# Kernel tuning notes

Hardware: AMD Instinct MI355X
Metric: run time of the kernel (lower is better)

## Reference

```python
import jax, jax.numpy as jnp
import numpy as np

ALPHA = 1.5      # entmax alpha (q parameter)
N_ITER = 50      # entmax-bisect iterations (entmax library default)
B, S, DM, H, HKV, HD = 1, 2048, 2048, 16, 4, 128
ROPE_THETA = 10000.0


def _entmax_p(x):
    """alpha-entmax along last axis via bisection on tau (matches entmax.EntmaxBisect)."""
    am1 = ALPHA - 1.0
    pw = 1.0 / am1
    X = x * am1
    d = x.shape[-1]
    max_val = jnp.max(X, axis=-1, keepdims=True)
    tau_lo = max_val - 1.0                      # _gp(1, alpha) = 1
    tau_hi = max_val - (1.0 / d) ** am1          # _gp(1/d, alpha)
    dm0 = tau_hi - tau_lo

    def body(i, carry):
        tau_lo, dm, tau_m = carry
        dm = dm * 0.5
        tau_m = tau_lo + dm
        p = jnp.maximum(X - tau_m, 0.0) ** pw
        f = jnp.sum(p, axis=-1, keepdims=True) - 1.0
        tau_lo = jnp.where(f >= 0, tau_m, tau_lo)
        return (tau_lo, dm, tau_m)

    tau_lo, dm, tau_m = jax.lax.fori_loop(0, N_ITER, body, (tau_lo, dm0, tau_lo))
    p = jnp.maximum(X - tau_m, 0.0) ** pw
    return p / jnp.sum(p, axis=-1, keepdims=True)  # ensure_sum_one


@jax.custom_vjp
def entmax_bisect(x):
    return _entmax_p(x)

def _emx_fwd(x):
    p = _entmax_p(x)
    return p, p

def _emx_bwd(p, g):
    # entmax library backward: gppr = p^(2-alpha) on support
    gppr = jnp.where(p > 0, p ** (2.0 - ALPHA), 0.0)
    dX = g * gppr
    q = jnp.sum(dX, axis=-1, keepdims=True) / jnp.sum(gppr, axis=-1, keepdims=True)
    return ((dX - q * gppr),)

entmax_bisect.defvjp(_emx_fwd, _emx_bwd)


def _rotate_half(x):
    x1, x2 = x[..., : HD // 2], x[..., HD // 2:]
    return jnp.concatenate([-x2, x1], axis=-1)


def setup_inputs() -> dict:
    key = jax.random.key(0)
    k1, k2, k3, k4, k5 = jax.random.split(key, 5)
    hidden_states = jax.random.normal(k1, (B, S, DM), dtype=jnp.float32)
    wq = jax.random.normal(k2, (H * HD, DM), dtype=jnp.float32) * 0.02
    wk = jax.random.normal(k3, (HKV * HD, DM), dtype=jnp.float32) * 0.02
    wv = jax.random.normal(k4, (HKV * HD, DM), dtype=jnp.float32) * 0.02
    wo = jax.random.normal(k5, (DM, H * HD), dtype=jnp.float32) * 0.02
    # real Llama RoPE position embeddings
    inv_freq = 1.0 / (ROPE_THETA ** (np.arange(0, HD, 2, dtype=np.float32) / HD))
    pos = np.arange(S, dtype=np.float32)
    freqs = pos[:, None] * inv_freq[None, :]          # [S, HD/2]
    emb = np.concatenate([freqs, freqs], axis=-1)     # [S, HD]
    cos = jnp.asarray(np.cos(emb))[None]              # [1, S, HD]
    sin = jnp.asarray(np.sin(emb))[None]
    return {"hidden_states": hidden_states, "cos": cos, "sin": sin,
            "wq": wq, "wk": wk, "wv": wv, "wo": wo}


def reference(hidden_states, cos, sin, wq, wk, wv, wo):
    b, s, _ = hidden_states.shape
    scaling = HD ** -0.5
    # QKV projections -> [B, H, S, HD]
    q = (hidden_states @ wq.T).reshape(b, s, H, HD).transpose(0, 2, 1, 3)
    k = (hidden_states @ wk.T).reshape(b, s, HKV, HD).transpose(0, 2, 1, 3)
    v = (hidden_states @ wv.T).reshape(b, s, HKV, HD).transpose(0, 2, 1, 3)
    # RoPE (cos/sin broadcast over head axis)
    c, sn = cos[:, None, :, :], sin[:, None, :, :]
    q = q * c + _rotate_half(q) * sn
    k = k * c + _rotate_half(k) * sn
    # GQA: repeat kv heads
    g = H // HKV
    k = jnp.repeat(k, g, axis=1)
    v = jnp.repeat(v, g, axis=1)
    scores = jnp.einsum('bhqd,bhkd->bhqk', q, k) * scaling
    causal = jnp.tril(jnp.ones((s, s), dtype=bool))
    scores = jnp.where(causal, scores, -jnp.inf)
    attn = entmax_bisect(scores)                      # [B, H, S, S]
    out = jnp.einsum('bhqk,bhkd->bhqd', attn, v)
    out = out.transpose(0, 2, 1, 3).reshape(b, s, H * HD)
    out = out @ wo.T
    return (out, attn)
```

## Files before the change

### kernel.cpp

```cpp
#include <hip/hip_runtime.h>

typedef __bf16 bf16;
typedef __bf16 bf16x4 __attribute__((ext_vector_type(4)));
typedef __bf16 bf16x8 __attribute__((ext_vector_type(8)));
typedef float f32x4 __attribute__((ext_vector_type(4)));

#define S 2048
#define DM 2048
#define HD 128
#define H 16
#define NQKV 3072
#define N_ITER_DEV 32

__device__ __forceinline__ void gl2lds16(const void* g, void* l) {
    __builtin_amdgcn_global_load_lds(
        (const __attribute__((address_space(1))) void*)g,
        (__attribute__((address_space(3))) void*)l, 16, 0, 0);
}

__global__ void cvt_all(const float* __restrict__ hid, const float* __restrict__ wq,
                        const float* __restrict__ wk, const float* __restrict__ wv,
                        const float* __restrict__ wo, bf16* __restrict__ bh,
                        bf16* __restrict__ bqkv, bf16* __restrict__ bwo) {
    int i = blockIdx.x * blockDim.x + threadIdx.x;
    const float* src;
    bf16* dst;
    int off;
    if (i < 1048576) { src = hid; dst = bh; off = i; }
    else if (i < 2097152) { src = wq; dst = bqkv; off = i - 1048576; }
    else if (i < 2359296) { src = wk; dst = bqkv + 2048 * 2048; off = i - 2097152; }
    else if (i < 2621440) { src = wv; dst = bqkv + 2048 * 2048 + 512 * 2048; off = i - 2359296; }
    else { src = wo; dst = bwo; off = i - 2621440; }
    float4 f = ((const float4*)src)[off];
    bf16x4 o;
    o[0] = (bf16)f.x; o[1] = (bf16)f.y; o[2] = (bf16)f.z; o[3] = (bf16)f.w;
    ((bf16x4*)dst)[off] = o;
}

__global__ __launch_bounds__(256) void gemm128_bt(const bf16* __restrict__ A,
                                                  const bf16* __restrict__ B,
                                                  float* __restrict__ C, int Ndim, int K) {
    __shared__ bf16 As[128 * 32];
    __shared__ bf16 Bs[128 * 32];
    int m0 = blockIdx.x * 128, n0 = blockIdx.y * 128;
    int t = threadIdx.x;
    int l = t & 63, w = t >> 6;
    int lane16 = l & 15, quad = l >> 4;

    int c0 = (w * 2) * 64 + l;
    int c1 = c0 + 64;
    const bf16* Abase = A + (size_t)m0 * K;
    const bf16* Bbase = B + (size_t)n0 * K;

    int wm = (w & 1) * 64, wn = (w >> 1) * 64;
    f32x4 acc[4][4];
#pragma unroll
    for (int i = 0; i < 4; i++)
#pragma unroll
        for (int j = 0; j < 4; j++) acc[i][j] = (f32x4){0.f, 0.f, 0.f, 0.f};

    for (int k0 = 0; k0 < K; k0 += 32) {
        gl2lds16(Abase + (size_t)(c0 >> 2) * K + k0 + (c0 & 3) * 8, &As[(w * 2) * 512]);
        gl2lds16(Abase + (size_t)(c1 >> 2) * K + k0 + (c1 & 3) * 8, &As[(w * 2 + 1) * 512]);
        gl2lds16(Bbase + (size_t)(c0 >> 2) * K + k0 + (c0 & 3) * 8, &Bs[(w * 2) * 512]);
        gl2lds16(Bbase + (size_t)(c1 >> 2) * K + k0 + (c1 & 3) * 8, &Bs[(w * 2 + 1) * 512]);
        __syncthreads();
        bf16x8 af[4], bfr[4];
#pragma unroll
        for (int i = 0; i < 4; i++)
            af[i] = *(const bf16x8*)&As[(wm + i * 16 + lane16) * 32 + quad * 8];
#pragma unroll
        for (int j = 0; j < 4; j++)
            bfr[j] = *(const bf16x8*)&Bs[(wn + j * 16 + lane16) * 32 + quad * 8];
#pragma unroll
        for (int i = 0; i < 4; i++)
#pragma unroll
            for (int j = 0; j < 4; j++)
                acc[i][j] = __builtin_amdgcn_mfma_f32_16x16x32_bf16(af[i], bfr[j], acc[i][j], 0, 0, 0);
        __syncthreads();
    }
#pragma unroll
    for (int i = 0; i < 4; i++)
#pragma unroll
        for (int j = 0; j < 4; j++) {
            float* cp = C + (size_t)(m0 + wm + i * 16 + quad * 4) * Ndim + n0 + wn + j * 16 + lane16;
#pragma unroll
            for (int r = 0; r < 4; r++) cp[(size_t)r * Ndim] = acc[i][j][r];
        }
}

__global__ void rope_kernel(const float* __restrict__ qkv, const float* __restrict__ cosb,
                            const float* __restrict__ sinb, bf16* __restrict__ qs,
                            bf16* __restrict__ kb, bf16* __restrict__ vT) {
    int col = blockIdx.x * 256 + threadIdx.x;
    int s = blockIdx.y;
    const float* row = qkv + (size_t)s * NQKV;
    float v = row[col];
    if (col < DM) {
        int h = col >> 7, d = col & 127;
        float c = cosb[s * HD + d], sn = sinb[s * HD + d];
        float other = row[(h << 7) + ((d < 64) ? (d + 64) : (d - 64))];
        float rot = (d < 64) ? -other : other;
        float o = v * c + rot * sn;
        qs[((size_t)h * S + s) * HD + d] = (bf16)(o * 0.04419417382415922f);
    } else if (col < DM + 512) {
        int c2 = col - DM;
        int kv = c2 >> 7, d = c2 & 127;
        float c = cosb[s * HD + d], sn = sinb[s * HD + d];
        float other = row[DM + (kv << 7) + ((d < 64) ? (d + 64) : (d - 64))];
        float rot = (d < 64) ? -other : other;
        float o = v * c + rot * sn;
        kb[((size_t)kv * S + s) * HD + d] = (bf16)o;
    } else {
        int c2 = col - DM - 512;
        int kv = c2 >> 7, d = c2 & 127;
        vT[((size_t)kv * HD + d) * S + s] = (bf16)v;
    }
}

template <int SEGS>
__global__ __launch_bounds__(1024) void attn_av_kernel(const bf16* __restrict__ qs,
                                                       const bf16* __restrict__ kb,
                                                       const bf16* __restrict__ vT,
                                                       float* __restrict__ attn,
                                                       bf16* __restrict__ o, int bx_base) {
    constexpr int NREG = SEGS * 8;
    __shared__ float sc[16][528];
    __shared__ bf16 pb[16][552];
    int bx = bx_base + blockIdx.x;
    int h = blockIdx.y;
    int r0 = bx * 16;
    int jlen = r0 + 16;
    int l = threadIdx.x & 63;
    int w = threadIdx.x >> 6;
    int lane16 = l & 15, quad = l >> 4;

    const bf16* qrow = qs + ((size_t)h * S + (r0 + lane16)) * HD + quad * 8;
    bf16x8 afrag[4];
#pragma unroll
    for (int kc = 0; kc < 4; kc++) afrag[kc] = *(const bf16x8*)(qrow + kc * 32);

    const bf16* kbase = kb + (size_t)(h >> 2) * S * HD;
    const bf16* vbase = vT + (size_t)(h >> 2) * HD * S;
    float xr[NREG];
    int my_i = r0 + w;

#pragma unroll
    for (int sgi = 0; sgi < SEGS; sgi++) {
        int j0 = sgi * 512;
#pragma unroll
        for (int tt = 0; tt < 2; tt++) {
            int t = w + tt * 16;
            int jt = j0 + t * 16;
            if (jt < jlen) {
                f32x4 acc = {0.f, 0.f, 0.f, 0.f};
                const bf16* kp = kbase + (size_t)(jt + lane16) * HD + quad * 8;
#pragma unroll
                for (int kc = 0; kc < 4; kc++) {
                    bf16x8 b = *(const bf16x8*)(kp + kc * 32);
                    acc = __builtin_amdgcn_mfma_f32_16x16x32_bf16(afrag[kc], b, acc, 0, 0, 0);
                }
                int jj = jt + lane16;
#pragma unroll
                for (int r = 0; r < 4; r++) {
                    int rowi = quad * 4 + r;
                    float v = acc[r];
                    if (jj > r0 + rowi) v = -1e30f;
                    sc[rowi][t * 16 + lane16] = v;
                }
            }
        }
        __syncthreads();
#pragma unroll
        for (int c = 0; c < 8; c++) {
            int j = j0 + c * 64 + l;
            xr[sgi * 8 + c] = (j < jlen) ? sc[w][c * 64 + l] : -1e30f;
        }
        __syncthreads();
    }

    float m = -1e30f;
#pragma unroll
    for (int c = 0; c < NREG; c++) m = fmaxf(m, xr[c]);
#pragma unroll
    for (int off = 1; off < 64; off <<= 1) m = fmaxf(m, __shfl_xor(m, off));

    float tau_lo = m - 1.0f;
    float dmh = 0.97790291309f;
    float tau_m = tau_lo;
    for (int it = 0; it < N_ITER_DEV; it++) {
        dmh *= 0.5f;
        tau_m = tau_lo + dmh;
        float f = 0.f;
#pragma unroll
        for (int c = 0; c < NREG; c++) {
            float t = fmaxf(xr[c] - tau_m, 0.f);
            f = fmaf(t, t, f);
        }
#pragma unroll
        for (int off = 1; off < 64; off <<= 1) f += __shfl_xor(f, off);
        tau_lo = (f >= 1.0f) ? tau_m : tau_lo;
    }

    float ssum = 0.f;
#pragma unroll
    for (int c = 0; c < NREG; c++) {
        float t = fmaxf(xr[c] - tau_m, 0.f);
        ssum = fmaf(t, t, ssum);
    }
#pragma unroll
    for (int off = 1; off < 64; off <<= 1) ssum += __shfl_xor(ssum, off);
    float inv = 1.0f / ssum;

    float* arow = attn + ((size_t)h * S + my_i) * S;
    int jt_o = (w & 7) * 16;
    int kh = (w >> 3) * 256;
    f32x4 acc_o = {0.f, 0.f, 0.f, 0.f};

#pragma unroll
    for (int sgi = 0; sgi < SEGS; sgi++) {
        int j0 = sgi * 512;
#pragma unroll
        for (int c = 0; c < 8; c++) {
            float t = fmaxf(xr[sgi * 8 + c] - tau_m, 0.f);
            float p = t * t * inv;
            arow[j0 + c * 64 + l] = p;
            pb[w][c * 64 + l] = (bf16)p;
        }
        __syncthreads();
#pragma unroll
        for (int ks = 0; ks < 8; ks++) {
            int kk = kh + ks * 32;
            bf16x8 a = *(const bf16x8*)&pb[lane16][kk + quad * 8];
            bf16x8 b = *(const bf16x8*)(vbase + (size_t)(jt_o + lane16) * S + j0 + kk + quad * 8);
            acc_o = __builtin_amdgcn_mfma_f32_16x16x32_bf16(a, b, acc_o, 0, 0, 0);
        }
        __syncthreads();
    }

    for (int j = SEGS * 512 + l; j < S; j += 64) arow[j] = 0.f;

    if (w >= 8) {
#pragma unroll
        for (int r = 0; r < 4; r++) sc[w - 8][l * 4 + r] = acc_o[r];
    }
    __syncthreads();
    if (w < 8) {
        bf16* op = o + (size_t)(r0 + quad * 4) * DM + h * HD + jt_o + lane16;
#pragma unroll
        for (int r = 0; r < 4; r++) {
            float v = acc_o[r] + sc[w][l * 4 + r];
            op[(size_t)r * DM] = (bf16)v;
        }
    }
}

extern "C" void kernel_launch(void* const* d_in, const int* in_sizes, int n_in,
                              void* d_out, int out_size, void* d_ws, size_t ws_size,
                              hipStream_t stream) {
    const float* hidden = (const float*)d_in[0];
    const float* cosb   = (const float*)d_in[1];
    const float* sinb   = (const float*)d_in[2];
    const float* wq     = (const float*)d_in[3];
    const float* wk     = (const float*)d_in[4];
    const float* wv     = (const float*)d_in[5];
    const float* wo     = (const float*)d_in[6];
    char* ws = (char*)d_ws;
    bf16*  bf_hidden = (bf16*)(ws);
    bf16*  bf_wqkv   = (bf16*)(ws + 8388608);
    bf16*  bf_wo     = (bf16*)(ws + 20971520);
    float* qkv_raw   = (float*)(ws + 29360128);
    bf16*  qsb       = (bf16*)(ws + 54525952);
    bf16*  kbb       = (bf16*)(ws + 62914560);
    bf16*  vTb       = (bf16*)(ws + 65011712);
    float* out  = (float*)d_out;
    float* attn = out + 4194304;

    cvt_all<<<dim3(14336), 256, 0, stream>>>(hidden, wq, wk, wv, wo, bf_hidden, bf_wqkv, bf_wo);

    gemm128_bt<<<dim3(16, 24), 256, 0, stream>>>(bf_hidden, bf_wqkv, qkv_raw, NQKV, DM);

    rope_kernel<<<dim3(12, S), 256, 0, stream>>>(qkv_raw, cosb, sinb, qsb, kbb, vTb);

    attn_av_kernel<1><<<dim3(32, H), 1024, 0, stream>>>(qsb, kbb, vTb, attn, bf_hidden, 0);
    attn_av_kernel<2><<<dim3(32, H), 1024, 0, stream>>>(qsb, kbb, vTb, attn, bf_hidden, 32);
    attn_av_kernel<3><<<dim3(32, H), 1024, 0, stream>>>(qsb, kbb, vTb, attn, bf_hidden, 64);
    attn_av_kernel<4><<<dim3(32, H), 1024, 0, stream>>>(qsb, kbb, vTb, attn, bf_hidden, 96);

    gemm128_bt<<<dim3(16, 16), 256, 0, stream>>>(bf_hidden, bf_wo, out, DM, DM);
}
```

Baseline: 689.2 us.

## Merge attention launches with heaviest-first scheduling, vectorize stores, cut bisection iterations

Replaces the four per-segment attention launches with one kernel that dispatches on segment count and schedules the longest query blocks first, which removes tail idle time between launches. The V transpose moves into its own kernel with coalesced writes. Score loads, probability stores and zero-fill now use float4 accesses. The entmax bisection drops from 32 to 20 iterations, which cuts compute but loosens the threshold precision and may hurt accuracy.

```diff
diff --git a/kernel.cpp b/kernel.cpp
--- a/kernel.cpp
+++ b/kernel.cpp
@@ -10,7 +10,7 @@
 #define HD 128
 #define H 16
 #define NQKV 3072
-#define N_ITER_DEV 32
+#define N_ITER_DEV 20
 
 __device__ __forceinline__ void gl2lds16(const void* g, void* l) {
     __builtin_amdgcn_global_load_lds(
@@ -89,9 +89,9 @@
         }
 }
 
-__global__ void rope_kernel(const float* __restrict__ qkv, const float* __restrict__ cosb,
-                            const float* __restrict__ sinb, bf16* __restrict__ qs,
-                            bf16* __restrict__ kb, bf16* __restrict__ vT) {
+__global__ void rope_qk(const float* __restrict__ qkv, const float* __restrict__ cosb,
+                        const float* __restrict__ sinb, bf16* __restrict__ qs,
+                        bf16* __restrict__ kb) {
     int col = blockIdx.x * 256 + threadIdx.x;
     int s = blockIdx.y;
     const float* row = qkv + (size_t)s * NQKV;
@@ -103,7 +103,7 @@
         float rot = (d < 64) ? -other : other;
         float o = v * c + rot * sn;
         qs[((size_t)h * S + s) * HD + d] = (bf16)(o * 0.04419417382415922f);
-    } else if (col < DM + 512) {
+    } else {
         int c2 = col - DM;
         int kv = c2 >> 7, d = c2 & 127;
         float c = cosb[s * HD + d], sn = sinb[s * HD + d];
@@ -111,25 +111,22 @@
         float rot = (d < 64) ? -other : other;
         float o = v * c + rot * sn;
         kb[((size_t)kv * S + s) * HD + d] = (bf16)o;
-    } else {
-        int c2 = col - DM - 512;
-        int kv = c2 >> 7, d = c2 & 127;
-        vT[((size_t)kv * HD + d) * S + s] = (bf16)v;
-    }
+    }
+}
+
+__global__ void vtrans(const float* __restrict__ qkv, bf16* __restrict__ vT) {
+    int s = blockIdx.x * 256 + threadIdx.x;
+    int y = blockIdx.y;
+    float v = qkv[(size_t)s * NQKV + 2560 + y];
+    vT[(size_t)y * S + s] = (bf16)v;
 }
 
 template <int SEGS>
-__global__ __launch_bounds__(1024) void attn_av_kernel(const bf16* __restrict__ qs,
-                                                       const bf16* __restrict__ kb,
-                                                       const bf16* __restrict__ vT,
-                                                       float* __restrict__ attn,
-                                                       bf16* __restrict__ o, int bx_base) {
+__device__ __forceinline__ void attn_body(const bf16* __restrict__ qs, const bf16* __restrict__ kb,
+                                          const bf16* __restrict__ vT, float* __restrict__ attn,
+                                          bf16* __restrict__ o, int r0, int h,
+                                          float (&sc)[16][528], bf16 (&pb)[16][552]) {
     constexpr int NREG = SEGS * 8;
-    __shared__ float sc[16][528];
-    __shared__ bf16 pb[16][552];
-    int bx = bx_base + blockIdx.x;
-    int h = blockIdx.y;
-    int r0 = bx * 16;
     int jlen = r0 + 16;
     int l = threadIdx.x & 63;
     int w = threadIdx.x >> 6;
@@ -143,7 +140,6 @@
     const bf16* kbase = kb + (size_t)(h >> 2) * S * HD;
     const bf16* vbase = vT + (size_t)(h >> 2) * HD * S;
     float xr[NREG];
-    int my_i = r0 + w;
 
 #pragma unroll
     for (int sgi = 0; sgi < SEGS; sgi++) {
@@ -172,9 +168,13 @@
         }
         __syncthreads();
 #pragma unroll
-        for (int c = 0; c < 8; c++) {
-            int j = j0 + c * 64 + l;
-            xr[sgi * 8 + c] = (j < jlen) ? sc[w][c * 64 + l] : -1e30f;
+        for (int part = 0; part < 2; part++) {
+            float4 f = *(const float4*)&sc[w][part * 256 + l * 4];
+            int jb = j0 + part * 256 + l * 4;
+            xr[sgi * 8 + part * 4 + 0] = (jb + 0 < jlen) ? f.x : -1e30f;
+            xr[sgi * 8 + part * 4 + 1] = (jb + 1 < jlen) ? f.y : -1e30f;
+            xr[sgi * 8 + part * 4 + 2] = (jb + 2 < jlen) ? f.z : -1e30f;
+            xr[sgi * 8 + part * 4 + 3] = (jb + 3 < jlen) ? f.w : -1e30f;
         }
         __syncthreads();
     }
@@ -212,7 +212,7 @@
     for (int off = 1; off < 64; off <<= 1) ssum += __shfl_xor(ssum, off);
     float inv = 1.0f / ssum;
 
-    float* arow = attn + ((size_t)h * S + my_i) * S;
+    float* arow = attn + ((size_t)h * S + (r0 + w)) * S;
     int jt_o = (w & 7) * 16;
     int kh = (w >> 3) * 256;
     f32x4 acc_o = {0.f, 0.f, 0.f, 0.f};
@@ -221,11 +221,18 @@
     for (int sgi = 0; sgi < SEGS; sgi++) {
         int j0 = sgi * 512;
 #pragma unroll
-        for (int c = 0; c < 8; c++) {
-            float t = fmaxf(xr[sgi * 8 + c] - tau_m, 0.f);
-            float p = t * t * inv;
-            arow[j0 + c * 64 + l] = p;
-            pb[w][c * 64 + l] = (bf16)p;
+        for (int part = 0; part < 2; part++) {
+            float4 pv;
+            float t0 = fmaxf(xr[sgi * 8 + part * 4 + 0] - tau_m, 0.f);
+            float t1 = fmaxf(xr[sgi * 8 + part * 4 + 1] - tau_m, 0.f);
+            float t2 = fmaxf(xr[sgi * 8 + part * 4 + 2] - tau_m, 0.f);
+            float t3 = fmaxf(xr[sgi * 8 + part * 4 + 3] - tau_m, 0.f);
+            pv.x = t0 * t0 * inv; pv.y = t1 * t1 * inv;
+            pv.z = t2 * t2 * inv; pv.w = t3 * t3 * inv;
+            *(float4*)&arow[j0 + part * 256 + l * 4] = pv;
+            bf16x4 pbv;
+            pbv[0] = (bf16)pv.x; pbv[1] = (bf16)pv.y; pbv[2] = (bf16)pv.z; pbv[3] = (bf16)pv.w;
+            *(bf16x4*)&pb[w][part * 256 + l * 4] = pbv;
         }
         __syncthreads();
 #pragma unroll
@@ -238,7 +245,8 @@
         __syncthreads();
     }
 
-    for (int j = SEGS * 512 + l; j < S; j += 64) arow[j] = 0.f;
+    float4 z4 = {0.f, 0.f, 0.f, 0.f};
+    for (int j = SEGS * 512 + l * 4; j < S; j += 256) *(float4*)&arow[j] = z4;
 
     if (w >= 8) {
 #pragma unroll
@@ -252,6 +260,25 @@
             float v = acc_o[r] + sc[w][l * 4 + r];
             op[(size_t)r * DM] = (bf16)v;
         }
+    }
+}
+
+__global__ __launch_bounds__(1024) void attn_av_all(const bf16* __restrict__ qs,
+                                                    const bf16* __restrict__ kb,
+                                                    const bf16* __restrict__ vT,
+                                                    float* __restrict__ attn,
+                                                    bf16* __restrict__ o) {
+    __shared__ float sc[16][528];
+    __shared__ bf16 pb[16][552];
+    int qb = 127 - blockIdx.x;
+    int h = blockIdx.y;
+    int r0 = qb * 16;
+    int nseg = (qb >> 5) + 1;
+    switch (nseg) {
+        case 1: attn_body<1>(qs, kb, vT, attn, o, r0, h, sc, pb); break;
+        case 2: attn_body<2>(qs, kb, vT, attn, o, r0, h, sc, pb); break;
+        case 3: attn_body<3>(qs, kb, vT, attn, o, r0, h, sc, pb); break;
+        default: attn_body<4>(qs, kb, vT, attn, o, r0, h, sc, pb); break;
     }
 }
 
@@ -280,12 +307,10 @@
 
     gemm128_bt<<<dim3(16, 24), 256, 0, stream>>>(bf_hidden, bf_wqkv, qkv_raw, NQKV, DM);
 
-    rope_kernel<<<dim3(12, S), 256, 0, stream>>>(qkv_raw, cosb, sinb, qsb, kbb, vTb);
-
-    attn_av_kernel<1><<<dim3(32, H), 1024, 0, stream>>>(qsb, kbb, vTb, attn, bf_hidden, 0);
-    attn_av_kernel<2><<<dim3(32, H), 1024, 0, stream>>>(qsb, kbb, vTb, attn, bf_hidden, 32);
-    attn_av_kernel<3><<<dim3(32, H), 1024, 0, stream>>>(qsb, kbb, vTb, attn, bf_hidden, 64);
-    attn_av_kernel<4><<<dim3(32, H), 1024, 0, stream>>>(qsb, kbb, vTb, attn, bf_hidden, 96);
+    rope_qk<<<dim3(10, S), 256, 0, stream>>>(qkv_raw, cosb, sinb, qsb, kbb);
+    vtrans<<<dim3(8, 512), 256, 0, stream>>>(qkv_raw, vTb);
+
+    attn_av_all<<<dim3(128, H), 1024, 0, stream>>>(qsb, kbb, vTb, attn, bf_hidden);
 
     gemm128_bt<<<dim3(16, 16), 256, 0, stream>>>(bf_hidden, bf_wo, out, DM, DM);
 }
```

New measurement: 739.4 us. 1.07x slower.
